# Performance work log

Measured on AMD Instinct MI355X. Metric: run time of the kernel, lower is better.

The kernel has to match this reference:

```python
import jax, jax.numpy as jnp
import numpy as np

S = 192          # spatial_size
N = 100000       # active input sites
CIN, M, M2, NCLS = 3, 32, 64, 50
EPS = 1e-4       # scn BatchNorm eps
OFFS = np.array([[dx, dy, dz] for dx in (-1, 0, 1) for dy in (-1, 0, 1) for dz in (-1, 0, 1)], dtype=np.int64)


def _build_nbr(coords, size):
    # coords: [n,3] unique int64. Returns [n,27] int32 neighbor index (-1 = inactive site),
    # i.e. the submanifold-convolution rulebook built via sorted-key hashing.
    n = coords.shape[0]
    keys = (coords[:, 0] * size + coords[:, 1]) * size + coords[:, 2]
    order = np.argsort(keys)
    sk = keys[order]
    nbr = np.full((n, 27), -1, dtype=np.int32)
    for k, off in enumerate(OFFS):
        nc = coords + off
        ok = np.all((nc >= 0) & (nc < size), axis=1)
        qk = (nc[:, 0] * size + nc[:, 1]) * size + nc[:, 2]
        pos = np.searchsorted(sk, qk).clip(0, n - 1)
        hit = ok & (sk[pos] == qk)
        nbr[hit, k] = order[pos[hit]].astype(np.int32)
    return nbr


def setup_inputs() -> dict:
    rng = np.random.default_rng(0)
    raw = rng.integers(0, S, size=(130000, 3), dtype=np.int64)
    keys = (raw[:, 0] * S + raw[:, 1]) * S + raw[:, 2]
    _, first = np.unique(keys, return_index=True)
    coords = raw[np.sort(first)][:N]          # N unique active voxels
    nbr_fine = _build_nbr(coords, S)
    # stride-2 / filter-2 downsample rulebook: coarse sites = unique(coords // 2)
    S2 = S // 2
    cc = coords // 2
    ckeys = (cc[:, 0] * S2 + cc[:, 1]) * S2 + cc[:, 2]
    uk, parent = np.unique(ckeys, return_inverse=True)
    ccoords = np.column_stack((uk // (S2 * S2), (uk // S2) % S2, uk % S2))
    nbr_coarse = _build_nbr(ccoords, S2)
    offset_id = (coords[:, 0] % 2) * 4 + (coords[:, 1] % 2) * 2 + coords[:, 2] % 2
    key = jax.random.key(0)
    ks = jax.random.split(key, 8)
    def w(k, shape, fan):
        return jax.random.normal(k, shape, jnp.float32) * (1.0 / np.sqrt(fan))
    return dict(
        coords=jnp.asarray(coords, jnp.int32),
        features=jax.random.normal(ks[0], (N, CIN), jnp.float32),
        nbr_fine=jnp.asarray(nbr_fine),
        nbr_coarse=jnp.asarray(nbr_coarse),
        parent=jnp.asarray(parent.astype(np.int32)),
        offset_id=jnp.asarray(offset_id.astype(np.int32)),
        num_coarse=int(uk.shape[0]),
        w_in=w(ks[1], (27, CIN, M), 27 * CIN),
        w_b1=w(ks[2], (27, M, M), 27 * M),
        w_down=w(ks[3], (8, M, M2), 8 * M),
        w_b2=w(ks[4], (27, M2, M2), 27 * M2),
        w_up=w(ks[5], (8, M2, M), 8 * M2),
        w_b3=w(ks[6], (27, 2 * M, M), 27 * 2 * M),
        g1=jnp.ones((M,)), b1=jnp.zeros((M,)),
        gd=jnp.ones((M,)), bd=jnp.zeros((M,)),
        g2=jnp.ones((M2,)), b2=jnp.zeros((M2,)),
        gu=jnp.ones((M2,)), bu=jnp.zeros((M2,)),
        g3=jnp.ones((2 * M,)), b3=jnp.zeros((2 * M,)),
        go=jnp.ones((M,)), bo=jnp.zeros((M,)),
        w_lin=w(ks[7], (M, NCLS), M),
        b_lin=jnp.zeros((NCLS,)),
    )


def _subm_conv(f, nbr, W):
    # f: [n,Cin], nbr: [n,27] (-1 = inactive), W: [27,Cin,Cout]
    mask = nbr >= 0
    g = f[jnp.where(mask, nbr, 0)] * mask[..., None]  # [n,27,Cin]
    return jnp.einsum('nkc,kcd->nd', g, W)


def _bnrelu(f, gamma, beta):
    mu = f.mean(0)
    var = ((f - mu) ** 2).mean(0)
    return jax.nn.relu((f - mu) * (gamma / jnp.sqrt(var + EPS)) + beta)


def _down(f, parent, off_id, W, nc):
    # strided 2^3 conv: out[parent] += W[offset(child)] @ f[child]
    out = jnp.zeros((nc, W.shape[2]), f.dtype)
    for o in range(8):
        sel = (off_id == o)[:, None].astype(f.dtype)
        out = out + jax.ops.segment_sum((f * sel) @ W[o], parent, num_segments=nc)
    return out


def _up(g, parent, off_id, W):
    # 2^3 deconv back to fine sites
    gp = g[parent]
    out = jnp.zeros((gp.shape[0], W.shape[2]), g.dtype)
    for o in range(8):
        out = out + (off_id == o)[:, None].astype(g.dtype) * (gp @ W[o])
    return out


def reference(coords, features, nbr_fine, nbr_coarse, parent, offset_id, num_coarse,
              w_in, w_b1, w_down, w_b2, w_up, w_b3,
              g1, b1, gd, bd, g2, b2, gu, bu, g3, b3, go, bo, w_lin, b_lin):
    # InputLayer (coords unique -> identity) + SubmanifoldConvolution(CIN->M)
    f = _subm_conv(features, nbr_fine, w_in)
    # UNet level 0 block (pre-activation)
    f = _subm_conv(_bnrelu(f, g1, b1), nbr_fine, w_b1)
    skip = f
    # downsample: BNReLU + Convolution(M->M2, 2, 2)
    g = _down(_bnrelu(f, gd, bd), parent, offset_id, w_down, num_coarse)
    # UNet level 1 block
    g = _subm_conv(_bnrelu(g, g2, b2), nbr_coarse, w_b2)
    # upsample: BNReLU + Deconvolution(M2->M, 2, 2)
    u = _up(_bnrelu(g, gu, bu), parent, offset_id, w_up)
    # JoinTable + block (2M -> M)
    f = jnp.concatenate([skip, u], axis=1)
    f = _subm_conv(_bnrelu(f, g3, b3), nbr_fine, w_b3)
    # top-level BatchNormReLU(M) + OutputLayer + Linear head
    f = _bnrelu(f, go, bo)
    return f @ w_lin + b_lin
```

## Files before the change

### kernel.cpp

```cpp
#include <hip/hip_runtime.h>

#define EPS_BN 1e-4f
constexpr int BLK = 256;
constexpr int ECAPC = 1856;
constexpr int NCOPY = 8;

__global__ __launch_bounds__(64) void build_fine_k(
    const int* __restrict__ nbr, int n, int* __restrict__ cnt, int* __restrict__ ent) {
  int i = blockIdx.x * 64 + threadIdx.x;
  if (i >= n) return;
  int c = 0;
  const int* nr = nbr + (size_t)i * 27;
  int* er = ent + (size_t)i * 27;
#pragma unroll 1
  for (int k = 0; k < 27; ++k) {
    int j = nr[k];
    if (j >= 0) er[c++] = (k << 18) | j;
  }
  cnt[i] = c;
}

__global__ __launch_bounds__(64) void build_subm4_k(
    const int* __restrict__ nbr, int n,
    int* __restrict__ segP, int* __restrict__ ent) {
  int T = blockIdx.x, r = threadIdx.x;
  int i = T * 64 + r;
  bool valid = i < n;
  int base = 0;
#pragma unroll 1
  for (int k = 0; k < 27; ++k) {
    int j = valid ? nbr[(size_t)i * 27 + k] : -1;
    bool act = j >= 0;
    unsigned long long mb = __ballot(act);
    int cnt = __popcll(mb);
    int pre = __popcll(mb & ((1ull << r) - 1));
    if (act) ent[(size_t)T * ECAPC + base + pre] = (r << 23) | (k << 18) | j;
    int padded = (cnt + 3) & ~3;
    if (r < padded - cnt) ent[(size_t)T * ECAPC + base + cnt + r] = -1;
    base += padded;
  }
  if (r == 0) segP[T] = base;
}

__global__ __launch_bounds__(BLK) void child_scatter_k(
    const int* __restrict__ parent, const int* __restrict__ offid, int n,
    int* __restrict__ ccnt, int* __restrict__ cent) {
  int i = blockIdx.x * BLK + threadIdx.x;
  if (i >= n) return;
  int p = parent[i];
  int slot = atomicAdd(&ccnt[p], 1);
  cent[p * 8 + slot] = i | (offid[i] << 25);
}

template <int CI, int CO, int MODE>
__global__ __launch_bounds__(BLK) void tconvA_k(
    const float* __restrict__ in, const int* __restrict__ ent, const int* __restrict__ cnt,
    const int* __restrict__ parent, const int* __restrict__ offid,
    const float* __restrict__ W, float* __restrict__ out, int n,
    float* __restrict__ osums) {
  constexpr int LANES = CO / 4, SLOTS = BLK / LANES, RPS = 64 / SLOTS;
  __shared__ float red[2 * CO];
  int t = threadIdx.x;
  for (int idx = t; idx < 2 * CO; idx += BLK) red[idx] = 0.f;
  __syncthreads();
  int slot = t / LANES, lane = t % LANES, g = lane * 4;
  int T = blockIdx.x;
  float ssum[4] = {0, 0, 0, 0}, ssq[4] = {0, 0, 0, 0};
#pragma unroll 1
  for (int rr = 0; rr < RPS; ++rr) {
    int row = T * 64 + slot * RPS + rr;
    bool vrow = row < n;
    float a0 = 0.f, a1 = 0.f, a2 = 0.f, a3 = 0.f;
    int ec = 0;
    if (vrow) ec = (MODE == 2) ? 1 : cnt[row];
#pragma unroll 1
    for (int e = 0; e < ec; ++e) {
      int k, j;
      if constexpr (MODE == 0) {
        int v = ent[(size_t)row * 27 + e];
        k = (v >> 18) & 31; j = v & 0x3FFFF;
      } else if constexpr (MODE == 1) {
        int v = ent[(size_t)row * 8 + e];
        k = v >> 25; j = v & 0x1FFFFFF;
      } else {
        k = offid[row]; j = parent[row];
      }
      const float* Wk = W + (size_t)k * (CI * CO) + g;
      const float* xr = in + (size_t)j * CI;
#pragma unroll
      for (int h = 0; h < CI / 32; ++h) {
        float4 xv[8];
#pragma unroll
        for (int c4 = 0; c4 < 8; ++c4)
          xv[c4] = *reinterpret_cast<const float4*>(xr + h * 32 + c4 * 4);
#pragma unroll
        for (int c4 = 0; c4 < 8; ++c4) {
          float xs[4] = {xv[c4].x, xv[c4].y, xv[c4].z, xv[c4].w};
#pragma unroll
          for (int q = 0; q < 4; ++q) {
            float4 wv = *reinterpret_cast<const float4*>(Wk + (size_t)(h * 32 + c4 * 4 + q) * CO);
            a0 = fmaf(xs[q], wv.x, a0);
            a1 = fmaf(xs[q], wv.y, a1);
            a2 = fmaf(xs[q], wv.z, a2);
            a3 = fmaf(xs[q], wv.w, a3);
          }
        }
      }
    }
    if (vrow)
      *reinterpret_cast<float4*>(out + (size_t)row * CO + g) = make_float4(a0, a1, a2, a3);
    ssum[0] += a0; ssum[1] += a1; ssum[2] += a2; ssum[3] += a3;
    ssq[0] = fmaf(a0, a0, ssq[0]); ssq[1] = fmaf(a1, a1, ssq[1]);
    ssq[2] = fmaf(a2, a2, ssq[2]); ssq[3] = fmaf(a3, a3, ssq[3]);
  }
#pragma unroll
  for (int q = 0; q < 4; ++q) {
    atomicAdd(&red[g + q], ssum[q]);
    atomicAdd(&red[CO + g + q], ssq[q]);
  }
  __syncthreads();
  int copy = blockIdx.x & (NCOPY - 1);
  if (t < 2 * CO) atomicAdd(&osums[copy * 2 * CO + t], red[t]);
}

template <int CI, int CO>
__global__ __launch_bounds__(BLK) void tconvB_k(
    const float* __restrict__ in, const int* __restrict__ segP,
    const int* __restrict__ ent, int ecap,
    const float* __restrict__ W, float* __restrict__ out, int n,
    float* __restrict__ osums) {
  constexpr int GO = CO / 16;
  constexpr int AP = CO + 4;
  __shared__ float lacc[64 * AP];
  int t = threadIdx.x, T = blockIdx.x;
  for (int idx = t; idx < 64 * AP; idx += BLK) lacc[idx] = 0.f;
  __syncthreads();
  int P = segP[T];
  const int* entT = ent + (size_t)T * ecap;
  int slot = t >> 4, g = (t & 15) * GO;
#pragma unroll 1
  for (int pb = slot * 4; pb < P; pb += 64) {
    int ee[4] = {entT[pb], entT[pb + 1], entT[pb + 2], entT[pb + 3]};
    int k = (ee[0] >> 18) & 31;
    const float* Wk = W + (size_t)k * (CI * CO);
    float acc[4][GO];
#pragma unroll
    for (int pp = 0; pp < 4; ++pp)
#pragma unroll
      for (int b = 0; b < GO; ++b) acc[pp][b] = 0.f;
#pragma unroll 4
    for (int c4 = 0; c4 < CI / 4; ++c4) {
      int cb = c4 * 4;
      float xs[4][4];
#pragma unroll
      for (int pp = 0; pp < 4; ++pp) {
        float4 x = make_float4(0.f, 0.f, 0.f, 0.f);
        if (ee[pp] >= 0) {
          int j = ee[pp] & 0x3FFFF;
          x = *reinterpret_cast<const float4*>(in + (size_t)j * CI + cb);
        }
        xs[pp][0] = x.x; xs[pp][1] = x.y; xs[pp][2] = x.z; xs[pp][3] = x.w;
      }
#pragma unroll
      for (int q = 0; q < 4; ++q) {
        float4 w4 = *reinterpret_cast<const float4*>(Wk + (size_t)(cb + q) * CO + g);
        float wv[4] = {w4.x, w4.y, w4.z, w4.w};
#pragma unroll
        for (int pp = 0; pp < 4; ++pp)
#pragma unroll
          for (int b = 0; b < GO; ++b)
            acc[pp][b] = fmaf(xs[pp][q], wv[b], acc[pp][b]);
      }
    }
#pragma unroll
    for (int pp = 0; pp < 4; ++pp) {
      if (ee[pp] >= 0) {
        int r = (ee[pp] >> 23) & 63;
        float* ap = &lacc[r * AP + g];
#pragma unroll
        for (int b = 0; b < GO; ++b) atomicAdd(ap + b, acc[pp][b]);
      }
    }
  }
  __syncthreads();
  for (int idx = t; idx < 64 * (CO / 4); idx += BLK) {
    int r = idx / (CO / 4), c4 = idx - r * (CO / 4);
    int row = T * 64 + r;
    if (row < n)
      *reinterpret_cast<float4*>(out + (size_t)row * CO + c4 * 4) =
          *reinterpret_cast<const float4*>(&lacc[r * AP + c4 * 4]);
  }
  int copy = blockIdx.x & (NCOPY - 1);
  if (t < CO) {
    float s = 0.f, ss = 0.f;
#pragma unroll 4
    for (int r = 0; r < 64; ++r) {
      float x = lacc[r * AP + t];
      s += x; ss = fmaf(x, x, ss);
    }
    atomicAdd(&osums[copy * 2 * CO + t], s);
    atomicAdd(&osums[copy * 2 * CO + CO + t], ss);
  }
}

template <int C>
__global__ __launch_bounds__(BLK) void bnact_k(
    const float* __restrict__ in, const float* __restrict__ sums,
    const float* __restrict__ gm, const float* __restrict__ bt, float invn,
    float* __restrict__ outp, int n) {
  __shared__ float lst[2 * C];
  int t = threadIdx.x;
  if (t < C) {
    float s = 0.f, q = 0.f;
#pragma unroll
    for (int cp = 0; cp < NCOPY; ++cp) { s += sums[cp * 2 * C + t]; q += sums[cp * 2 * C + C + t]; }
    float mu = s * invn, var = q * invn - mu * mu;
    float sc = gm[t] / sqrtf(var + EPS_BN);
    lst[t] = sc; lst[C + t] = bt[t] - mu * sc;
  }
  __syncthreads();
  int total = n * (C / 4);
  const float4* in4 = reinterpret_cast<const float4*>(in);
  float4* out4 = reinterpret_cast<float4*>(outp);
  for (int idx = blockIdx.x * BLK + t; idx < total; idx += gridDim.x * BLK) {
    int cb = (idx & (C / 4 - 1)) * 4;
    float4 x = in4[idx];
    float v[4] = {x.x, x.y, x.z, x.w};
#pragma unroll
    for (int q = 0; q < 4; ++q) {
      float y = fmaf(v[q], lst[cb + q], lst[C + cb + q]);
      v[q] = y > 0.f ? y : 0.f;
    }
    out4[idx] = make_float4(v[0], v[1], v[2], v[3]);
  }
}

__global__ __launch_bounds__(BLK) void bncat_k(
    const float* __restrict__ fa, const float* __restrict__ sA,
    const float* __restrict__ gA, const float* __restrict__ bA,
    const float* __restrict__ fb, const float* __restrict__ sB,
    const float* __restrict__ gB, const float* __restrict__ bB,
    float invn, float* __restrict__ acat, int n) {
  __shared__ float lst[128];
  int t = threadIdx.x;
  if (t < 64) {
    int half = t >> 5, c = t & 31;
    const float* ss = half ? sB : sA;
    const float* gg = half ? gB : gA;
    const float* bb = half ? bB : bA;
    float s = 0.f, q = 0.f;
#pragma unroll
    for (int cp = 0; cp < NCOPY; ++cp) { s += ss[cp * 64 + c]; q += ss[cp * 64 + 32 + c]; }
    float mu = s * invn, var = q * invn - mu * mu;
    float sc = gg[c] / sqrtf(var + EPS_BN);
    lst[half * 64 + c] = sc; lst[half * 64 + 32 + c] = bb[c] - mu * sc;
  }
  __syncthreads();
  int total = n * 16;
  for (int idx = blockIdx.x * BLK + t; idx < total; idx += gridDim.x * BLK) {
    int row = idx >> 4, c4 = idx & 15;
    int half = c4 >> 3, cc = (c4 & 7) * 4;
    const float* src = half ? fb : fa;
    float4 x = *reinterpret_cast<const float4*>(src + (size_t)row * 32 + cc);
    const float* L = lst + half * 64;
    float v[4] = {x.x, x.y, x.z, x.w};
#pragma unroll
    for (int q = 0; q < 4; ++q) {
      float y = fmaf(v[q], L[cc + q], L[32 + cc + q]);
      v[q] = y > 0.f ? y : 0.f;
    }
    *reinterpret_cast<float4*>(acat + (size_t)row * 64 + c4 * 4) = make_float4(v[0], v[1], v[2], v[3]);
  }
}

__global__ __launch_bounds__(BLK) void conv_in_k(
    const float* __restrict__ feat, const int* __restrict__ nbr,
    const float* __restrict__ W, float* __restrict__ out, int n,
    float* __restrict__ osums) {
  int i = blockIdx.x * BLK + threadIdx.x;
  bool valid = i < n;
  float acc[32];
#pragma unroll
  for (int c = 0; c < 32; ++c) acc[c] = 0.f;
#pragma unroll 1
  for (int k = 0; k < 27; ++k) {
    int j = valid ? nbr[(size_t)i * 27 + k] : -1;
    if (j < 0) continue;
    float x0 = feat[j * 3 + 0], x1 = feat[j * 3 + 1], x2 = feat[j * 3 + 2];
    const float* w0 = W + k * 96;
#pragma unroll
    for (int co = 0; co < 8; ++co) {
      float4 a = *reinterpret_cast<const float4*>(w0 + co * 4);
      float4 b = *reinterpret_cast<const float4*>(w0 + 32 + co * 4);
      float4 cc = *reinterpret_cast<const float4*>(w0 + 64 + co * 4);
      acc[4*co+0] = fmaf(x0, a.x, fmaf(x1, b.x, fmaf(x2, cc.x, acc[4*co+0])));
      acc[4*co+1] = fmaf(x0, a.y, fmaf(x1, b.y, fmaf(x2, cc.y, acc[4*co+1])));
      acc[4*co+2] = fmaf(x0, a.z, fmaf(x1, b.z, fmaf(x2, cc.z, acc[4*co+2])));
      acc[4*co+3] = fmaf(x0, a.w, fmaf(x1, b.w, fmaf(x2, cc.w, acc[4*co+3])));
    }
  }
  if (valid) {
    float* o = out + (size_t)i * 32;
#pragma unroll
    for (int co = 0; co < 8; ++co)
      *reinterpret_cast<float4*>(o + co * 4) = make_float4(acc[4*co], acc[4*co+1], acc[4*co+2], acc[4*co+3]);
  }
  __shared__ float red[2][4][32];
  int w = threadIdx.x >> 6;
#pragma unroll
  for (int c = 0; c < 32; ++c) {
    float v = acc[c], q = acc[c] * acc[c];
#pragma unroll
    for (int off = 32; off; off >>= 1) {
      v += __shfl_down(v, off);
      q += __shfl_down(q, off);
    }
    if ((threadIdx.x & 63) == 0) { red[0][w][c] = v; red[1][w][c] = q; }
  }
  __syncthreads();
  if (threadIdx.x < 64) {
    int kind = threadIdx.x >> 5, c = threadIdx.x & 31;
    float s = red[kind][0][c] + red[kind][1][c] + red[kind][2][c] + red[kind][3][c];
    atomicAdd(&osums[(blockIdx.x & (NCOPY - 1)) * 64 + kind * 32 + c], s);
  }
}

__global__ __launch_bounds__(BLK) void head_k(
    const float* __restrict__ fin, const float* __restrict__ sums,
    const float* __restrict__ gm, const float* __restrict__ bt, float inv_n,
    const float* __restrict__ Wl, const float* __restrict__ bl,
    float* __restrict__ out, int n) {
  __shared__ float lw[32 * 50];
  __shared__ float lb[52];
  __shared__ float lst[64];
  int t = threadIdx.x;
  if (t < 32) {
    float s = 0.f, q = 0.f;
#pragma unroll
    for (int cp = 0; cp < NCOPY; ++cp) { s += sums[cp * 64 + t]; q += sums[cp * 64 + 32 + t]; }
    float mu = s * inv_n, var = q * inv_n - mu * mu;
    float sc = gm[t] / sqrtf(var + EPS_BN);
    lst[t] = sc; lst[32 + t] = bt[t] - mu * sc;
  }
  for (int idx = t; idx < 1600; idx += BLK) lw[idx] = Wl[idx];
  if (t < 50) lb[t] = bl[t];
  __syncthreads();
  int i = blockIdx.x * BLK + t;
  if (i >= n) return;
  float x[32];
  const float* fj = fin + (size_t)i * 32;
#pragma unroll
  for (int c4 = 0; c4 < 8; ++c4) {
    float4 v = *reinterpret_cast<const float4*>(fj + c4 * 4);
    float vs[4] = {v.x, v.y, v.z, v.w};
#pragma unroll
    for (int q = 0; q < 4; ++q) {
      int c = c4 * 4 + q;
      float y = fmaf(vs[q], lst[c], lst[32 + c]);
      x[c] = y > 0.f ? y : 0.f;
    }
  }
  float acc[50];
#pragma unroll
  for (int co = 0; co < 50; ++co) acc[co] = lb[co];
#pragma unroll 4
  for (int c = 0; c < 32; ++c) {
#pragma unroll
    for (int co = 0; co < 50; ++co) acc[co] = fmaf(x[c], lw[c * 50 + co], acc[co]);
  }
  float* o = out + (size_t)i * 50;
#pragma unroll
  for (int co = 0; co < 25; ++co)
    *reinterpret_cast<float2*>(o + co * 2) = make_float2(acc[co * 2], acc[co * 2 + 1]);
}

extern "C" void kernel_launch(void* const* d_in, const int* in_sizes, int n_in,
                              void* d_out, int out_size, void* d_ws, size_t ws_size,
                              hipStream_t stream) {
  const float* feat   = (const float*)d_in[1];
  const int*   nbrF   = (const int*)d_in[2];
  const int*   nbrC   = (const int*)d_in[3];
  const int*   parent = (const int*)d_in[4];
  const int*   offid  = (const int*)d_in[5];
  const float* w_in   = (const float*)d_in[7];
  const float* w_b1   = (const float*)d_in[8];
  const float* w_down = (const float*)d_in[9];
  const float* w_b2   = (const float*)d_in[10];
  const float* w_up   = (const float*)d_in[11];
  const float* w_b3   = (const float*)d_in[12];
  const float* g1v = (const float*)d_in[13], *b1v = (const float*)d_in[14];
  const float* gdv = (const float*)d_in[15], *bdv = (const float*)d_in[16];
  const float* g2v = (const float*)d_in[17], *b2v = (const float*)d_in[18];
  const float* guv = (const float*)d_in[19], *buv = (const float*)d_in[20];
  const float* g3v = (const float*)d_in[21], *b3v = (const float*)d_in[22];
  const float* gov = (const float*)d_in[23], *bov = (const float*)d_in[24];
  const float* w_lin = (const float*)d_in[25];
  const float* b_lin = (const float*)d_in[26];
  float* out = (float*)d_out;

  int N  = in_sizes[4];
  int NC = in_sizes[3] / 27;
  int ntF = (N + 63) / 64, ntC = (NC + 63) / 64;

  size_t szF = (size_t)N * 32;
  size_t szG = (size_t)NC * 64;
  size_t SB  = (size_t)N * 64;

  float* ws = (float*)d_ws;
  float* S1 = ws;
  float* S2 = S1 + SB;
  float* S3 = S2 + SB;
  float* S4 = S3 + szF;
  float* S5 = S4 + szF;
  float* sums1 = S5 + szG;
  float* sumsD = sums1 + 8 * 64;
  float* sums2 = sumsD + 8 * 64;
  float* sumsU = sums2 + 8 * 128;
  float* sums4 = sumsU + 8 * 128;
  float* sums5 = sums4 + 8 * 64;
  int* ccnt = (int*)(sums5 + 8 * 64);
  int* cent = ccnt + NC;
  int* cntF = cent + (size_t)NC * 8;
  int* entF = cntF + N;
  int* segPC = entF + (size_t)N * 27;
  int* entC  = segPC + ntC;

  hipMemsetAsync(sums1, 0, (4096 + NC) * sizeof(float), stream);

  int gridN = (N + BLK - 1) / BLK;
  int agrid = 1024;
  float invN = 1.f / (float)N, invC = 1.f / (float)NC;

  build_fine_k<<<ntF, 64, 0, stream>>>(nbrF, N, cntF, entF);
  build_subm4_k<<<ntC, 64, 0, stream>>>(nbrC, NC, segPC, entC);
  child_scatter_k<<<gridN, BLK, 0, stream>>>(parent, offid, N, ccnt, cent);

  conv_in_k<<<gridN, BLK, 0, stream>>>(feat, nbrF, w_in, S1, N, sums1);
  bnact_k<32><<<agrid, BLK, 0, stream>>>(S1, sums1, g1v, b1v, invN, S2, N);

  tconvA_k<32, 32, 0><<<ntF, BLK, 0, stream>>>(
      S2, entF, cntF, nullptr, nullptr, w_b1, S3, N, sumsD);
  bnact_k<32><<<agrid, BLK, 0, stream>>>(S3, sumsD, gdv, bdv, invN, S4, N);

  tconvA_k<32, 64, 1><<<ntC, BLK, 0, stream>>>(
      S4, cent, ccnt, nullptr, nullptr, w_down, S5, NC, sums2);
  bnact_k<64><<<agrid, BLK, 0, stream>>>(S5, sums2, g2v, b2v, invC, S2, NC);

  tconvB_k<64, 64><<<ntC, BLK, 0, stream>>>(
      S2, segPC, entC, ECAPC, w_b2, S1, NC, sumsU);
  bnact_k<64><<<agrid, BLK, 0, stream>>>(S1, sumsU, guv, buv, invC, S5, NC);

  tconvA_k<64, 32, 2><<<ntF, BLK, 0, stream>>>(
      S5, nullptr, nullptr, parent, offid, w_up, S4, N, sums4);

  bncat_k<<<agrid, BLK, 0, stream>>>(
      S3, sumsD, g3v, b3v, S4, sums4, g3v + 32, b3v + 32, invN, S2, N);

  tconvA_k<64, 32, 0><<<ntF, BLK, 0, stream>>>(
      S2, entF, cntF, nullptr, nullptr, w_b3, S3, N, sums5);

  head_k<<<gridN, BLK, 0, stream>>>(S3, sums5, gov, bov, invN, w_lin, b_lin, out, N);
}
```

Before: 586.6 us.

## Fuse BatchNorm+ReLU into conv input loads and stage tconvB inputs in LDS

Removes the standalone bnact/bncat passes by computing the BN scale/shift per block and applying BN+ReLU as each conv gathers its input rows, including reading the two concat halves from separate buffers. This drops several full read/write sweeps over activations. In exchange, the affine+ReLU is recomputed for every neighbor gather (up to 27 times per row), adding ALU work to gather-heavy kernels. tconvB additionally double-buffers normalized gathered rows through shared memory per wave, which adds LDS footprint and may lower occupancy.

```diff
diff --git a/kernel.cpp b/kernel.cpp
--- a/kernel.cpp
+++ b/kernel.cpp
@@ -32,11 +32,11 @@
     int j = valid ? nbr[(size_t)i * 27 + k] : -1;
     bool act = j >= 0;
     unsigned long long mb = __ballot(act);
-    int cnt = __popcll(mb);
+    int cntk = __popcll(mb);
     int pre = __popcll(mb & ((1ull << r) - 1));
     if (act) ent[(size_t)T * ECAPC + base + pre] = (r << 23) | (k << 18) | j;
-    int padded = (cnt + 3) & ~3;
-    if (r < padded - cnt) ent[(size_t)T * ECAPC + base + cnt + r] = -1;
+    int padded = (cntk + 3) & ~3;
+    if (r < padded - cntk) ent[(size_t)T * ECAPC + base + cntk + r] = -1;
     base += padded;
   }
   if (r == 0) segP[T] = base;
@@ -52,17 +52,37 @@
   cent[p * 8 + slot] = i | (offid[i] << 25);
 }
 
-template <int CI, int CO, int MODE>
+template <int CI, int CO, int MODE, bool CAT>
 __global__ __launch_bounds__(BLK) void tconvA_k(
-    const float* __restrict__ in, const int* __restrict__ ent, const int* __restrict__ cnt,
+    const float* __restrict__ inA, const float* __restrict__ inB,
+    const int* __restrict__ ent, const int* __restrict__ cnt,
     const int* __restrict__ parent, const int* __restrict__ offid,
+    const float* __restrict__ sumsA, const float* __restrict__ sumsB,
+    const float* __restrict__ gm, const float* __restrict__ bt, float invn,
     const float* __restrict__ W, float* __restrict__ out, int n,
     float* __restrict__ osums) {
   constexpr int LANES = CO / 4, SLOTS = BLK / LANES, RPS = 64 / SLOTS;
+  constexpr int CIA = CAT ? CI / 2 : CI;
   __shared__ float red[2 * CO];
+  __shared__ float lst[2 * CI];
   int t = threadIdx.x;
+  if (t < CI) {
+    float s = 0.f, q = 0.f;
+    if (!CAT || t < CI / 2) {
+#pragma unroll
+      for (int cp = 0; cp < NCOPY; ++cp) { s += sumsA[cp * 2 * CIA + t]; q += sumsA[cp * 2 * CIA + CIA + t]; }
+    } else {
+      int c = t - CI / 2;
+#pragma unroll
+      for (int cp = 0; cp < NCOPY; ++cp) { s += sumsB[cp * 2 * CIA + c]; q += sumsB[cp * 2 * CIA + CIA + c]; }
+    }
+    float mu = s * invn, var = q * invn - mu * mu;
+    float sc = gm[t] / sqrtf(var + EPS_BN);
+    lst[t] = sc; lst[CI + t] = bt[t] - mu * sc;
+  }
   for (int idx = t; idx < 2 * CO; idx += BLK) red[idx] = 0.f;
   __syncthreads();
+
   int slot = t / LANES, lane = t % LANES, g = lane * 4;
   int T = blockIdx.x;
   float ssum[4] = {0, 0, 0, 0}, ssq[4] = {0, 0, 0, 0};
@@ -86,23 +106,33 @@
         k = offid[row]; j = parent[row];
       }
       const float* Wk = W + (size_t)k * (CI * CO) + g;
-      const float* xr = in + (size_t)j * CI;
 #pragma unroll
       for (int h = 0; h < CI / 32; ++h) {
+        const float* xr;
+        if constexpr (CAT) xr = (h == 0 ? inA : inB) + (size_t)j * CIA;
+        else xr = inA + (size_t)j * CI + h * 32;
         float4 xv[8];
 #pragma unroll
         for (int c4 = 0; c4 < 8; ++c4)
-          xv[c4] = *reinterpret_cast<const float4*>(xr + h * 32 + c4 * 4);
+          xv[c4] = *reinterpret_cast<const float4*>(xr + c4 * 4);
 #pragma unroll
         for (int c4 = 0; c4 < 8; ++c4) {
-          float xs[4] = {xv[c4].x, xv[c4].y, xv[c4].z, xv[c4].w};
+          int cb = h * 32 + c4 * 4;
+          float4 sc4 = *reinterpret_cast<const float4*>(&lst[cb]);
+          float4 sh4 = *reinterpret_cast<const float4*>(&lst[CI + cb]);
+          float xs[4];
+          xs[0] = fmaf(xv[c4].x, sc4.x, sh4.x);
+          xs[1] = fmaf(xv[c4].y, sc4.y, sh4.y);
+          xs[2] = fmaf(xv[c4].z, sc4.z, sh4.z);
+          xs[3] = fmaf(xv[c4].w, sc4.w, sh4.w);
 #pragma unroll
           for (int q = 0; q < 4; ++q) {
-            float4 wv = *reinterpret_cast<const float4*>(Wk + (size_t)(h * 32 + c4 * 4 + q) * CO);
-            a0 = fmaf(xs[q], wv.x, a0);
-            a1 = fmaf(xs[q], wv.y, a1);
-            a2 = fmaf(xs[q], wv.z, a2);
-            a3 = fmaf(xs[q], wv.w, a3);
+            float x = xs[q] > 0.f ? xs[q] : 0.f;
+            float4 wv = *reinterpret_cast<const float4*>(Wk + (size_t)(cb + q) * CO);
+            a0 = fmaf(x, wv.x, a0);
+            a1 = fmaf(x, wv.y, a1);
+            a2 = fmaf(x, wv.z, a2);
+            a3 = fmaf(x, wv.w, a3);
           }
         }
       }
@@ -127,62 +157,129 @@
 __global__ __launch_bounds__(BLK) void tconvB_k(
     const float* __restrict__ in, const int* __restrict__ segP,
     const int* __restrict__ ent, int ecap,
+    const float* __restrict__ sums, const float* __restrict__ gm,
+    const float* __restrict__ bt, float invn,
     const float* __restrict__ W, float* __restrict__ out, int n,
     float* __restrict__ osums) {
   constexpr int GO = CO / 16;
   constexpr int AP = CO + 4;
   __shared__ float lacc[64 * AP];
+  __shared__ float lxs[4][2][16 * CI];
+  __shared__ int   lxe[4][2][16];
+  __shared__ float lst[2 * CI];
   int t = threadIdx.x, T = blockIdx.x;
+  if (t < CI) {
+    float s = 0.f, q = 0.f;
+#pragma unroll
+    for (int cp = 0; cp < NCOPY; ++cp) { s += sums[cp * 2 * CI + t]; q += sums[cp * 2 * CI + CI + t]; }
+    float mu = s * invn, var = q * invn - mu * mu;
+    float sc = gm[t] / sqrtf(var + EPS_BN);
+    lst[t] = sc; lst[CI + t] = bt[t] - mu * sc;
+  }
   for (int idx = t; idx < 64 * AP; idx += BLK) lacc[idx] = 0.f;
   __syncthreads();
+
   int P = segP[T];
   const int* entT = ent + (size_t)T * ecap;
-  int slot = t >> 4, g = (t & 15) * GO;
-#pragma unroll 1
-  for (int pb = slot * 4; pb < P; pb += 64) {
-    int ee[4] = {entT[pb], entT[pb + 1], entT[pb + 2], entT[pb + 3]};
-    int k = (ee[0] >> 18) & 31;
-    const float* Wk = W + (size_t)k * (CI * CO);
-    float acc[4][GO];
-#pragma unroll
-    for (int pp = 0; pp < 4; ++pp)
-#pragma unroll
-      for (int b = 0; b < GO; ++b) acc[pp][b] = 0.f;
+  int w = t >> 6, l = t & 63;
+  int pr = l >> 2, cq = l & 3;
+  int sw = l >> 4, g = (l & 15) * GO;
+  float* lx0 = lxs[w][0]; float* lx1 = lxs[w][1];
+  int* le0 = lxe[w][0];   int* le1 = lxe[w][1];
+  int ebase = w * 16;
+
+  auto stageLoad = [&](int base, float4 xq[4], int& e16o, int& epo) {
+    e16o = entT[base + (l & 15)];
+    epo = entT[base + pr];
+    int j = epo >= 0 ? (epo & 0x3FFFF) : 0;
+    const float* xr = in + (size_t)j * CI + cq * 16;
+#pragma unroll
+    for (int q = 0; q < 4; ++q) xq[q] = *reinterpret_cast<const float4*>(xr + q * 4);
+  };
+  auto stageWrite = [&](float* lxn, int* lxen, const float4 xq[4], int e16, int ep) {
+    if (l < 16) lxen[l] = e16;
+#pragma unroll
+    for (int q = 0; q < 4; ++q) {
+      int cb = cq * 16 + q * 4;
+      float4 sc4 = *reinterpret_cast<const float4*>(&lst[cb]);
+      float4 sh4 = *reinterpret_cast<const float4*>(&lst[CI + cb]);
+      float v0 = fmaf(xq[q].x, sc4.x, sh4.x);
+      float v1 = fmaf(xq[q].y, sc4.y, sh4.y);
+      float v2 = fmaf(xq[q].z, sc4.z, sh4.z);
+      float v3 = fmaf(xq[q].w, sc4.w, sh4.w);
+      v0 = (ep >= 0 && v0 > 0.f) ? v0 : 0.f;
+      v1 = (ep >= 0 && v1 > 0.f) ? v1 : 0.f;
+      v2 = (ep >= 0 && v2 > 0.f) ? v2 : 0.f;
+      v3 = (ep >= 0 && v3 > 0.f) ? v3 : 0.f;
+      *reinterpret_cast<float4*>(&lxn[pr * CI + cb]) = make_float4(v0, v1, v2, v3);
+    }
+  };
+
+  if (ebase < P) {
+    float4 xq[4]; int e16, ep;
+    stageLoad(ebase, xq, e16, ep);
+    stageWrite(lx0, le0, xq, e16, ep);
+  }
+  int cur = 0;
+#pragma unroll 1
+  for (int eb = ebase; eb < P; eb += 64) {
+    int ebn = eb + 64;
+    bool hasnext = ebn < P;
+    float4 xq[4]; int e16n = -1, epn = -1;
+    if (hasnext) stageLoad(ebn, xq, e16n, epn);
+    const float* lxc = cur ? lx1 : lx0;
+    const int* lxec = cur ? le1 : le0;
+    if (eb + sw * 4 < P) {
+      int e0 = lxec[sw * 4];
+      int k = (e0 >> 18) & 31;
+      const float* Wk = W + (size_t)k * (CI * CO) + g;
+      int rr4[4];
+      float acc[4][GO];
+#pragma unroll
+      for (int pp = 0; pp < 4; ++pp) {
+        int ev = lxec[sw * 4 + pp];
+        rr4[pp] = ev >= 0 ? ((ev >> 23) & 63) : -1;
+#pragma unroll
+        for (int b = 0; b < GO; ++b) acc[pp][b] = 0.f;
+      }
 #pragma unroll 4
-    for (int c4 = 0; c4 < CI / 4; ++c4) {
-      int cb = c4 * 4;
-      float xs[4][4];
+      for (int c4 = 0; c4 < CI / 4; ++c4) {
+        int cb = c4 * 4;
+        float xs[4][4];
+#pragma unroll
+        for (int pp = 0; pp < 4; ++pp) {
+          float4 xv = *reinterpret_cast<const float4*>(&lxc[(sw * 4 + pp) * CI + cb]);
+          xs[pp][0] = xv.x; xs[pp][1] = xv.y; xs[pp][2] = xv.z; xs[pp][3] = xv.w;
+        }
+#pragma unroll
+        for (int q = 0; q < 4; ++q) {
+          float4 w4 = *reinterpret_cast<const float4*>(Wk + (size_t)(cb + q) * CO);
+          float wv[4] = {w4.x, w4.y, w4.z, w4.w};
+#pragma unroll
+          for (int pp = 0; pp < 4; ++pp)
+#pragma unroll
+            for (int b = 0; b < GO; ++b)
+              acc[pp][b] = fmaf(xs[pp][q], wv[b], acc[pp][b]);
+        }
+      }
 #pragma unroll
       for (int pp = 0; pp < 4; ++pp) {
-        float4 x = make_float4(0.f, 0.f, 0.f, 0.f);
-        if (ee[pp] >= 0) {
-          int j = ee[pp] & 0x3FFFF;
-          x = *reinterpret_cast<const float4*>(in + (size_t)j * CI + cb);
+        if (rr4[pp] >= 0) {
+          float* ap = &lacc[rr4[pp] * AP + g];
+#pragma unroll
+          for (int b = 0; b < GO; ++b) atomicAdd(ap + b, acc[pp][b]);
         }
-        xs[pp][0] = x.x; xs[pp][1] = x.y; xs[pp][2] = x.z; xs[pp][3] = x.w;
       }
-#pragma unroll
-      for (int q = 0; q < 4; ++q) {
-        float4 w4 = *reinterpret_cast<const float4*>(Wk + (size_t)(cb + q) * CO + g);
-        float wv[4] = {w4.x, w4.y, w4.z, w4.w};
-#pragma unroll
-        for (int pp = 0; pp < 4; ++pp)
-#pragma unroll
-          for (int b = 0; b < GO; ++b)
-            acc[pp][b] = fmaf(xs[pp][q], wv[b], acc[pp][b]);
-      }
-    }
-#pragma unroll
-    for (int pp = 0; pp < 4; ++pp) {
-      if (ee[pp] >= 0) {
-        int r = (ee[pp] >> 23) & 63;
-        float* ap = &lacc[r * AP + g];
-#pragma unroll
-        for (int b = 0; b < GO; ++b) atomicAdd(ap + b, acc[pp][b]);
-      }
-    }
-  }
-  __syncthreads();
+    }
+    if (hasnext) {
+      float* lxn = cur ? lx0 : lx1;
+      int* lxen = cur ? le0 : le1;
+      stageWrite(lxn, lxen, xq, e16n, epn);
+    }
+    cur ^= 1;
+  }
+  __syncthreads();
+
   for (int idx = t; idx < 64 * (CO / 4); idx += BLK) {
     int r = idx / (CO / 4), c4 = idx - r * (CO / 4);
     int row = T * 64 + r;
@@ -200,76 +297,6 @@
     }
     atomicAdd(&osums[copy * 2 * CO + t], s);
     atomicAdd(&osums[copy * 2 * CO + CO + t], ss);
-  }
-}
-
-template <int C>
-__global__ __launch_bounds__(BLK) void bnact_k(
-    const float* __restrict__ in, const float* __restrict__ sums,
-    const float* __restrict__ gm, const float* __restrict__ bt, float invn,
-    float* __restrict__ outp, int n) {
-  __shared__ float lst[2 * C];
-  int t = threadIdx.x;
-  if (t < C) {
-    float s = 0.f, q = 0.f;
-#pragma unroll
-    for (int cp = 0; cp < NCOPY; ++cp) { s += sums[cp * 2 * C + t]; q += sums[cp * 2 * C + C + t]; }
-    float mu = s * invn, var = q * invn - mu * mu;
-    float sc = gm[t] / sqrtf(var + EPS_BN);
-    lst[t] = sc; lst[C + t] = bt[t] - mu * sc;
-  }
-  __syncthreads();
-  int total = n * (C / 4);
-  const float4* in4 = reinterpret_cast<const float4*>(in);
-  float4* out4 = reinterpret_cast<float4*>(outp);
-  for (int idx = blockIdx.x * BLK + t; idx < total; idx += gridDim.x * BLK) {
-    int cb = (idx & (C / 4 - 1)) * 4;
-    float4 x = in4[idx];
-    float v[4] = {x.x, x.y, x.z, x.w};
-#pragma unroll
-    for (int q = 0; q < 4; ++q) {
-      float y = fmaf(v[q], lst[cb + q], lst[C + cb + q]);
-      v[q] = y > 0.f ? y : 0.f;
-    }
-    out4[idx] = make_float4(v[0], v[1], v[2], v[3]);
-  }
-}
-
-__global__ __launch_bounds__(BLK) void bncat_k(
-    const float* __restrict__ fa, const float* __restrict__ sA,
-    const float* __restrict__ gA, const float* __restrict__ bA,
-    const float* __restrict__ fb, const float* __restrict__ sB,
-    const float* __restrict__ gB, const float* __restrict__ bB,
-    float invn, float* __restrict__ acat, int n) {
-  __shared__ float lst[128];
-  int t = threadIdx.x;
-  if (t < 64) {
-    int half = t >> 5, c = t & 31;
-    const float* ss = half ? sB : sA;
-    const float* gg = half ? gB : gA;
-    const float* bb = half ? bB : bA;
-    float s = 0.f, q = 0.f;
-#pragma unroll
-    for (int cp = 0; cp < NCOPY; ++cp) { s += ss[cp * 64 + c]; q += ss[cp * 64 + 32 + c]; }
-    float mu = s * invn, var = q * invn - mu * mu;
-    float sc = gg[c] / sqrtf(var + EPS_BN);
-    lst[half * 64 + c] = sc; lst[half * 64 + 32 + c] = bb[c] - mu * sc;
-  }
-  __syncthreads();
-  int total = n * 16;
-  for (int idx = blockIdx.x * BLK + t; idx < total; idx += gridDim.x * BLK) {
-    int row = idx >> 4, c4 = idx & 15;
-    int half = c4 >> 3, cc = (c4 & 7) * 4;
-    const float* src = half ? fb : fa;
-    float4 x = *reinterpret_cast<const float4*>(src + (size_t)row * 32 + cc);
-    const float* L = lst + half * 64;
-    float v[4] = {x.x, x.y, x.z, x.w};
-#pragma unroll
-    for (int q = 0; q < 4; ++q) {
-      float y = fmaf(v[q], L[cc + q], L[32 + cc + q]);
-      v[q] = y > 0.f ? y : 0.f;
-    }
-    *reinterpret_cast<float4*>(acat + (size_t)row * 64 + c4 * 4) = make_float4(v[0], v[1], v[2], v[3]);
   }
 }
 
@@ -402,17 +429,11 @@
   int NC = in_sizes[3] / 27;
   int ntF = (N + 63) / 64, ntC = (NC + 63) / 64;
 
-  size_t szF = (size_t)N * 32;
-  size_t szG = (size_t)NC * 64;
-  size_t SB  = (size_t)N * 64;
-
   float* ws = (float*)d_ws;
-  float* S1 = ws;
-  float* S2 = S1 + SB;
-  float* S3 = S2 + SB;
-  float* S4 = S3 + szF;
-  float* S5 = S4 + szF;
-  float* sums1 = S5 + szG;
+  float* B1 = ws;
+  float* B2 = B1 + (size_t)N * 64;
+  float* B3 = B2 + (size_t)N * 32;
+  float* sums1 = B3 + (size_t)N * 64;
   float* sumsD = sums1 + 8 * 64;
   float* sums2 = sumsD + 8 * 64;
   float* sumsU = sums2 + 8 * 128;
@@ -428,36 +449,32 @@
   hipMemsetAsync(sums1, 0, (4096 + NC) * sizeof(float), stream);
 
   int gridN = (N + BLK - 1) / BLK;
-  int agrid = 1024;
   float invN = 1.f / (float)N, invC = 1.f / (float)NC;
 
   build_fine_k<<<ntF, 64, 0, stream>>>(nbrF, N, cntF, entF);
   build_subm4_k<<<ntC, 64, 0, stream>>>(nbrC, NC, segPC, entC);
   child_scatter_k<<<gridN, BLK, 0, stream>>>(parent, offid, N, ccnt, cent);
 
-  conv_in_k<<<gridN, BLK, 0, stream>>>(feat, nbrF, w_in, S1, N, sums1);
-  bnact_k<32><<<agrid, BLK, 0, stream>>>(S1, sums1, g1v, b1v, invN, S2, N);
-
-  tconvA_k<32, 32, 0><<<ntF, BLK, 0, stream>>>(
-      S2, entF, cntF, nullptr, nullptr, w_b1, S3, N, sumsD);
-  bnact_k<32><<<agrid, BLK, 0, stream>>>(S3, sumsD, gdv, bdv, invN, S4, N);
-
-  tconvA_k<32, 64, 1><<<ntC, BLK, 0, stream>>>(
-      S4, cent, ccnt, nullptr, nullptr, w_down, S5, NC, sums2);
-  bnact_k<64><<<agrid, BLK, 0, stream>>>(S5, sums2, g2v, b2v, invC, S2, NC);
+  conv_in_k<<<gridN, BLK, 0, stream>>>(feat, nbrF, w_in, B1, N, sums1);
+
+  tconvA_k<32, 32, 0, false><<<ntF, BLK, 0, stream>>>(
+      B1, nullptr, entF, cntF, nullptr, nullptr,
+      sums1, nullptr, g1v, b1v, invN, w_b1, B2, N, sumsD);
+
+  tconvA_k<32, 64, 1, false><<<ntC, BLK, 0, stream>>>(
+      B2, nullptr, cent, ccnt, nullptr, nullptr,
+      sumsD, nullptr, gdv, bdv, invN, w_down, B3, NC, sums2);
 
   tconvB_k<64, 64><<<ntC, BLK, 0, stream>>>(
-      S2, segPC, entC, ECAPC, w_b2, S1, NC, sumsU);
-  bnact_k<64><<<agrid, BLK, 0, stream>>>(S1, sumsU, guv, buv, invC, S5, NC);
-
-  tconvA_k<64, 32, 2><<<ntF, BLK, 0, stream>>>(
-      S5, nullptr, nullptr, parent, offid, w_up, S4, N, sums4);
-
-  bncat_k<<<agrid, BLK, 0, stream>>>(
-      S3, sumsD, g3v, b3v, S4, sums4, g3v + 32, b3v + 32, invN, S2, N);
-
-  tconvA_k<64, 32, 0><<<ntF, BLK, 0, stream>>>(
-      S2, entF, cntF, nullptr, nullptr, w_b3, S3, N, sums5);
-
-  head_k<<<gridN, BLK, 0, stream>>>(S3, sums5, gov, bov, invN, w_lin, b_lin, out, N);
-}
+      B3, segPC, entC, ECAPC, sums2, g2v, b2v, invC, w_b2, B1, NC, sumsU);
+
+  tconvA_k<64, 32, 2, false><<<ntF, BLK, 0, stream>>>(
+      B1, nullptr, nullptr, nullptr, parent, offid,
+      sumsU, nullptr, guv, buv, invC, w_up, B3, N, sums4);
+
+  tconvA_k<64, 32, 0, true><<<ntF, BLK, 0, stream>>>(
+      B2, B3, entF, cntF, nullptr, nullptr,
+      sumsD, sums4, g3v, b3v, invN, w_b3, B1, N, sums5);
+
+  head_k<<<gridN, BLK, 0, stream>>>(B1, sums5, gov, bov, invN, w_lin, b_lin, out, N);
+}
```

Result: slower. 678.1 us (+15.6%).

## Fuse BN-ReLU into coarse subm conv and stage gathered rows in shared memory

Applied to the files above, without the earlier changes.

Drops the separate batchnorm+ReLU pass before the coarse submanifold convolution. The conv kernel now computes the scale and shift from the partial sums and applies them while gathering neighbor rows. Gathered inputs are staged in 128-entry chunks in shared memory instead of each thread reading global rows inside the inner loop. This removes one full read and write pass over the coarse activations. In exchange it adds extra barriers per chunk and recomputes the activation once per neighbor rather than once per site (about 27 times as many).

```diff
diff --git a/kernel.cpp b/kernel.cpp
--- a/kernel.cpp
+++ b/kernel.cpp
@@ -32,11 +32,11 @@
     int j = valid ? nbr[(size_t)i * 27 + k] : -1;
     bool act = j >= 0;
     unsigned long long mb = __ballot(act);
-    int cnt = __popcll(mb);
+    int cntk = __popcll(mb);
     int pre = __popcll(mb & ((1ull << r) - 1));
     if (act) ent[(size_t)T * ECAPC + base + pre] = (r << 23) | (k << 18) | j;
-    int padded = (cnt + 3) & ~3;
-    if (r < padded - cnt) ent[(size_t)T * ECAPC + base + cnt + r] = -1;
+    int padded = (cntk + 3) & ~3;
+    if (r < padded - cntk) ent[(size_t)T * ECAPC + base + cntk + r] = -1;
     base += padded;
   }
   if (r == 0) segP[T] = base;
@@ -127,62 +127,103 @@
 __global__ __launch_bounds__(BLK) void tconvB_k(
     const float* __restrict__ in, const int* __restrict__ segP,
     const int* __restrict__ ent, int ecap,
+    const float* __restrict__ sums, const float* __restrict__ gm,
+    const float* __restrict__ bt, float invn,
     const float* __restrict__ W, float* __restrict__ out, int n,
     float* __restrict__ osums) {
-  constexpr int GO = CO / 16;
-  constexpr int AP = CO + 4;
+  constexpr int AP = CO + 2;
+  constexpr int XP = CI + 2;
+  constexpr int CHUNK = 128;
   __shared__ float lacc[64 * AP];
+  __shared__ float lx[CHUNK * XP];
+  __shared__ int   lent[CHUNK];
+  __shared__ float lst[2 * CI];
   int t = threadIdx.x, T = blockIdx.x;
+  if (t < CI) {
+    float s = 0.f, q = 0.f;
+#pragma unroll
+    for (int cp = 0; cp < NCOPY; ++cp) { s += sums[cp * 2 * CI + t]; q += sums[cp * 2 * CI + CI + t]; }
+    float mu = s * invn, var = q * invn - mu * mu;
+    float sc = gm[t] / sqrtf(var + EPS_BN);
+    lst[t] = sc; lst[CI + t] = bt[t] - mu * sc;
+  }
   for (int idx = t; idx < 64 * AP; idx += BLK) lacc[idx] = 0.f;
-  __syncthreads();
   int P = segP[T];
   const int* entT = ent + (size_t)T * ecap;
-  int slot = t >> 4, g = (t & 15) * GO;
-#pragma unroll 1
-  for (int pb = slot * 4; pb < P; pb += 64) {
-    int ee[4] = {entT[pb], entT[pb + 1], entT[pb + 2], entT[pb + 3]};
-    int k = (ee[0] >> 18) & 31;
-    const float* Wk = W + (size_t)k * (CI * CO);
-    float acc[4][GO];
-#pragma unroll
-    for (int pp = 0; pp < 4; ++pp)
-#pragma unroll
-      for (int b = 0; b < GO; ++b) acc[pp][b] = 0.f;
+  int slot = t >> 4, g = (t & 15) * 4;
+  __syncthreads();
+
+#pragma unroll 1
+  for (int c0 = 0; c0 < P; c0 += CHUNK) {
+    int lim = min(P - c0, CHUNK);
+    if (t < CHUNK) lent[t] = (t < lim) ? entT[c0 + t] : -1;
+    for (int idx = t; idx < CHUNK * 16; idx += BLK) {
+      int pr = idx >> 4, cq = idx & 15;
+      int ev = (pr < lim) ? entT[c0 + pr] : -1;
+      float4 v = make_float4(0.f, 0.f, 0.f, 0.f);
+      if (ev >= 0) {
+        int j = ev & 0x3FFFF;
+        float4 x = *reinterpret_cast<const float4*>(in + (size_t)j * CI + cq * 4);
+        int cb = cq * 4;
+        float y0 = fmaf(x.x, lst[cb + 0], lst[CI + cb + 0]);
+        float y1 = fmaf(x.y, lst[cb + 1], lst[CI + cb + 1]);
+        float y2 = fmaf(x.z, lst[cb + 2], lst[CI + cb + 2]);
+        float y3 = fmaf(x.w, lst[cb + 3], lst[CI + cb + 3]);
+        v = make_float4(y0 > 0.f ? y0 : 0.f, y1 > 0.f ? y1 : 0.f,
+                        y2 > 0.f ? y2 : 0.f, y3 > 0.f ? y3 : 0.f);
+      }
+      *reinterpret_cast<float4*>(&lx[pr * XP + cq * 4]) = v;
+    }
+    __syncthreads();
+#pragma unroll 1
+    for (int gr = slot; gr * 4 < lim; gr += 16) {
+      int p0 = gr * 4;
+      int e0 = lent[p0];
+      int k = (e0 >> 18) & 31;
+      const float* Wk = W + (size_t)k * (CI * CO) + g;
+      int rr[4];
+      float acc[4][4];
+#pragma unroll
+      for (int pp = 0; pp < 4; ++pp) {
+        int ev = lent[p0 + pp];
+        rr[pp] = ev >= 0 ? ((ev >> 23) & 63) : -1;
+        acc[pp][0] = acc[pp][1] = acc[pp][2] = acc[pp][3] = 0.f;
+      }
 #pragma unroll 4
-    for (int c4 = 0; c4 < CI / 4; ++c4) {
-      int cb = c4 * 4;
-      float xs[4][4];
+      for (int c4 = 0; c4 < CI / 4; ++c4) {
+        int cb = c4 * 4;
+        float xs[4][4];
+#pragma unroll
+        for (int pp = 0; pp < 4; ++pp) {
+          float4 xv = *reinterpret_cast<const float4*>(&lx[(p0 + pp) * XP + cb]);
+          xs[pp][0] = xv.x; xs[pp][1] = xv.y; xs[pp][2] = xv.z; xs[pp][3] = xv.w;
+        }
+#pragma unroll
+        for (int q = 0; q < 4; ++q) {
+          float4 w4 = *reinterpret_cast<const float4*>(Wk + (size_t)(cb + q) * CO);
+#pragma unroll
+          for (int pp = 0; pp < 4; ++pp) {
+            acc[pp][0] = fmaf(xs[pp][q], w4.x, acc[pp][0]);
+            acc[pp][1] = fmaf(xs[pp][q], w4.y, acc[pp][1]);
+            acc[pp][2] = fmaf(xs[pp][q], w4.z, acc[pp][2]);
+            acc[pp][3] = fmaf(xs[pp][q], w4.w, acc[pp][3]);
+          }
+        }
+      }
 #pragma unroll
       for (int pp = 0; pp < 4; ++pp) {
-        float4 x = make_float4(0.f, 0.f, 0.f, 0.f);
-        if (ee[pp] >= 0) {
-          int j = ee[pp] & 0x3FFFF;
-          x = *reinterpret_cast<const float4*>(in + (size_t)j * CI + cb);
+        if (rr[pp] >= 0) {
+          float* ap = &lacc[rr[pp] * AP + g];
+          atomicAdd(ap + 0, acc[pp][0]);
+          atomicAdd(ap + 1, acc[pp][1]);
+          atomicAdd(ap + 2, acc[pp][2]);
+          atomicAdd(ap + 3, acc[pp][3]);
         }
-        xs[pp][0] = x.x; xs[pp][1] = x.y; xs[pp][2] = x.z; xs[pp][3] = x.w;
       }
-#pragma unroll
-      for (int q = 0; q < 4; ++q) {
-        float4 w4 = *reinterpret_cast<const float4*>(Wk + (size_t)(cb + q) * CO + g);
-        float wv[4] = {w4.x, w4.y, w4.z, w4.w};
-#pragma unroll
-        for (int pp = 0; pp < 4; ++pp)
-#pragma unroll
-          for (int b = 0; b < GO; ++b)
-            acc[pp][b] = fmaf(xs[pp][q], wv[b], acc[pp][b]);
-      }
-    }
-#pragma unroll
-    for (int pp = 0; pp < 4; ++pp) {
-      if (ee[pp] >= 0) {
-        int r = (ee[pp] >> 23) & 63;
-        float* ap = &lacc[r * AP + g];
-#pragma unroll
-        for (int b = 0; b < GO; ++b) atomicAdd(ap + b, acc[pp][b]);
-      }
-    }
-  }
-  __syncthreads();
+    }
+    __syncthreads();
+  }
+
   for (int idx = t; idx < 64 * (CO / 4); idx += BLK) {
     int r = idx / (CO / 4), c4 = idx - r * (CO / 4);
     int row = T * 64 + r;
@@ -444,10 +485,9 @@
 
   tconvA_k<32, 64, 1><<<ntC, BLK, 0, stream>>>(
       S4, cent, ccnt, nullptr, nullptr, w_down, S5, NC, sums2);
-  bnact_k<64><<<agrid, BLK, 0, stream>>>(S5, sums2, g2v, b2v, invC, S2, NC);
 
   tconvB_k<64, 64><<<ntC, BLK, 0, stream>>>(
-      S2, segPC, entC, ECAPC, w_b2, S1, NC, sumsU);
+      S5, segPC, entC, ECAPC, sums2, g2v, b2v, invC, w_b2, S1, NC, sumsU);
   bnact_k<64><<<agrid, BLK, 0, stream>>>(S1, sumsU, guv, buv, invC, S5, NC);
 
   tconvA_k<64, 32, 2><<<ntF, BLK, 0, stream>>>(
```

Result: faster. 552.8 us (-5.8%).
